# Kernel tuning notes

Hardware: AMD Instinct MI355X
Metric: run time of the kernel (lower is better)

Reference implementation:

```python
import jax, jax.numpy as jnp
import numpy as np

H = 768        # bert hidden_size
HID = 512      # lstm_hidden
HALF = HID // 2
T = 20         # tagset_size
START, STOP = 18, 19
S = 16386      # input positions incl. CLS/SEP
NEG = -10000.0


def setup_inputs() -> dict:
    key = jax.random.key(0)
    ks = jax.random.split(key, 12)
    sc_x = 1.0
    x = jax.random.normal(ks[0], (1, S, H), dtype=jnp.float32)
    # PyTorch LSTM params (gate order i,f,g,o), one layer, bidirectional
    s_ih = 1.0 / np.sqrt(HALF)
    w_ih_f = jax.random.uniform(ks[1], (4 * HALF, H), jnp.float32, -s_ih, s_ih)
    w_hh_f = jax.random.uniform(ks[2], (4 * HALF, HALF), jnp.float32, -s_ih, s_ih)
    b_ih_f = jax.random.uniform(ks[3], (4 * HALF,), jnp.float32, -s_ih, s_ih)
    b_hh_f = jax.random.uniform(ks[4], (4 * HALF,), jnp.float32, -s_ih, s_ih)
    w_ih_b = jax.random.uniform(ks[5], (4 * HALF, H), jnp.float32, -s_ih, s_ih)
    w_hh_b = jax.random.uniform(ks[6], (4 * HALF, HALF), jnp.float32, -s_ih, s_ih)
    b_ih_b = jax.random.uniform(ks[7], (4 * HALF,), jnp.float32, -s_ih, s_ih)
    b_hh_b = jax.random.uniform(ks[8], (4 * HALF,), jnp.float32, -s_ih, s_ih)
    s_t = 1.0 / np.sqrt(HID)
    w_tag = jax.random.uniform(ks[9], (T, HID), jnp.float32, -s_t, s_t)
    b_tag = jax.random.uniform(ks[10], (T,), jnp.float32, -s_t, s_t)
    transitions = jax.random.normal(ks[11], (T, T), dtype=jnp.float32)
    transitions = transitions.at[START, :].set(NEG).at[:, STOP].set(NEG)
    return {
        "x": x,
        "w_ih_f": w_ih_f, "w_hh_f": w_hh_f, "b_ih_f": b_ih_f, "b_hh_f": b_hh_f,
        "w_ih_b": w_ih_b, "w_hh_b": w_hh_b, "b_ih_b": b_ih_b, "b_hh_b": b_hh_b,
        "w_tag": w_tag, "b_tag": b_tag, "transitions": transitions,
    }


def _lstm_one_step(xt, w_ih, b_ih, b_hh):
    # Original passes [1, N, H] to a batch_first=False LSTM => seq_len=1,
    # batch=N, zero initial state. So each token does ONE cell step:
    # h0=c0=0 => hh contribution is only b_hh.
    g = xt @ w_ih.T + b_ih + b_hh          # [N, 4*HALF]
    i, f, gg, o = jnp.split(g, 4, axis=-1)  # PyTorch gate order i,f,g,o
    c = jax.nn.sigmoid(i) * jnp.tanh(gg)    # f*c0 = 0
    return jax.nn.sigmoid(o) * jnp.tanh(c)  # [N, HALF]


def reference(x, w_ih_f, w_hh_f, b_ih_f, b_hh_f,
              w_ih_b, w_hh_b, b_ih_b, b_hh_b,
              w_tag, b_tag, transitions):
    tok = x[0, 1:-1, :]                     # narrow(1,1,S-2): drop CLS/SEP -> [N,H]
    h_f = _lstm_one_step(tok, w_ih_f, b_ih_f, b_hh_f)
    h_b = _lstm_one_step(tok, w_ih_b, b_ih_b, b_hh_b)
    enc = jnp.concatenate([h_f, h_b], axis=-1)   # [N, HID]
    feats = enc @ w_tag.T + b_tag                # [N, T] emission scores

    # ---- Viterbi decode (sequential DP over tokens) ----
    init = jnp.full((T,), NEG, dtype=feats.dtype).at[START].set(0.0)

    def vstep(fv, feat):
        scores = fv[None, :] + transitions       # [next_tag, prev_tag]
        bp = jnp.argmax(scores, axis=1)          # backpointers [T]
        fv_new = jnp.max(scores, axis=1) + feat
        return fv_new, bp

    fv, bps = jax.lax.scan(vstep, init, feats)   # bps: [N, T]
    terminal = fv + transitions[STOP]
    best = jnp.argmax(terminal)
    path_score = terminal[best]

    def btrack(b, bp):
        return bp[b], b                          # emit tag at time t, move to t-1

    _, best_path = jax.lax.scan(btrack, best, bps, reverse=True)  # [N] in time order
    return path_score, best_path
```

## Files before the change

kernel.cpp:

```cpp
#include <hip/hip_runtime.h>
#include <math.h>

#define HDIM 768
#define HIDD 512
#define NTOK 16384
#define NT 20
#define CHUNKS 128
#define CLEN 128

typedef unsigned short ushort_t;
typedef __attribute__((ext_vector_type(8))) short bf16x8;
typedef __attribute__((ext_vector_type(4))) float f32x4;

__device__ __forceinline__ float sigm(float x){ return 1.0f/(1.0f+expf(-x)); }

__device__ __forceinline__ ushort_t f2bf(float f){
    unsigned int u = __float_as_uint(f);
    unsigned int r = (u + 0x7fffu + ((u >> 16) & 1u)) >> 16;
    return (ushort_t)r;
}
__device__ __forceinline__ float bf2f(ushort_t b){
    return __uint_as_float(((unsigned int)b) << 16);
}

#define GLD16(gp, lp) __builtin_amdgcn_global_load_lds( \
    (const __attribute__((address_space(1))) void*)(gp), \
    (__attribute__((address_space(3))) void*)(lp), 16, 0, 0)

__global__ __launch_bounds__(256) void conv_kernel(
    const float* __restrict__ x,
    const float* __restrict__ wf, const float* __restrict__ wb,
    ushort_t* __restrict__ Ah, ushort_t* __restrict__ Al,
    ushort_t* __restrict__ Bh, ushort_t* __restrict__ Bl)
{
    const int bid = blockIdx.x;
    if (bid < 1152){
        int t = bid*256 + threadIdx.x;
        int n = t / 192, c4 = (t - n*192)*4;
        int dir = n / 768, nr = n - dir*768;
        int gate = nr >> 8, j = nr & 255;
        int wrow = j + ((gate==0)?0:((gate==1)?512:768));
        const float* src = dir ? wb : wf;
        const float4 v = *(const float4*)(src + (size_t)wrow*HDIM + c4);
        float f[4] = {v.x, v.y, v.z, v.w};
        ushort_t h[4], l[4];
        #pragma unroll
        for (int i=0;i<4;++i){
            h[i] = f2bf(f[i]);
            l[i] = f2bf(f[i] - bf2f(h[i]));
        }
        *(ushort4*)(Bh + (size_t)n*HDIM + c4) = make_ushort4(h[0],h[1],h[2],h[3]);
        *(ushort4*)(Bl + (size_t)n*HDIM + c4) = make_ushort4(l[0],l[1],l[2],l[3]);
    } else {
        int t = (bid-1152)*256 + threadIdx.x;
        int row = t / 192, c4 = (t - row*192)*4;
        const float4 v = *(const float4*)(x + (size_t)(row+1)*HDIM + c4);
        float f[4] = {v.x, v.y, v.z, v.w};
        ushort_t h[4], l[4];
        #pragma unroll
        for (int i=0;i<4;++i){
            h[i] = f2bf(f[i]);
            l[i] = f2bf(f[i] - bf2f(h[i]));
        }
        *(ushort4*)(Ah + (size_t)row*HDIM + c4) = make_ushort4(h[0],h[1],h[2],h[3]);
        *(ushort4*)(Al + (size_t)row*HDIM + c4) = make_ushort4(l[0],l[1],l[2],l[3]);
    }
}

#define VMCNT(n) asm volatile("s_waitcnt vmcnt(" #n ")" ::: "memory")
#define BARRIER() asm volatile("s_barrier" ::: "memory")
#define LGKM0()  do{ asm volatile("s_waitcnt lgkmcnt(0)" ::: "memory"); \
                     __builtin_amdgcn_sched_barrier(0); }while(0)

#define READ_B(g, ab) do{                                                     \
    bfr[0] = *(const bf16x8*)((ab) + 16384 + (g)*16384 + boffB[0]);           \
    bfr[1] = *(const bf16x8*)((ab) + 16384 + (g)*16384 + 8192 + boffB[0]);    \
    bfr[2] = *(const bf16x8*)((ab) + 16384 + (g)*16384 + boffB[1]);           \
    bfr[3] = *(const bf16x8*)((ab) + 16384 + (g)*16384 + 8192 + boffB[1]);    \
}while(0)

#define READ_AH(S, ab) do{ _Pragma("unroll") for (int f=0; f<4; ++f)          \
    aH##S[f] = *(const bf16x8*)((ab) + aoffB[f]); }while(0)
#define READ_AL(ab) do{ _Pragma("unroll") for (int f=0; f<4; ++f)             \
    aL[f] = *(const bf16x8*)((ab) + 8192 + aoffB[f]); }while(0)

#define MFMA_CLUSTER(g, S) do{                                                \
  __builtin_amdgcn_s_setprio(1);                                              \
  _Pragma("unroll")                                                           \
  for (int fn=0; fn<2; ++fn){                                                 \
    _Pragma("unroll")                                                         \
    for (int fm=0; fm<4; ++fm){                                               \
      acc[g][fm][fn] = __builtin_amdgcn_mfma_f32_16x16x32_bf16(aH##S[fm],     \
          bfr[fn*2], acc[g][fm][fn], 0, 0, 0);                                \
      acc[g][fm][fn] = __builtin_amdgcn_mfma_f32_16x16x32_bf16(aL[fm],        \
          bfr[fn*2], acc[g][fm][fn], 0, 0, 0);                                \
      acc[g][fm][fn] = __builtin_amdgcn_mfma_f32_16x16x32_bf16(aH##S[fm],     \
          bfr[fn*2+1], acc[g][fm][fn], 0, 0, 0);                              \
    }                                                                         \
  }                                                                           \
  __builtin_amdgcn_s_setprio(0);                                              \
  __builtin_amdgcn_sched_barrier(0);                                          \
}while(0)

#define PH0(kt, P, CUR) do{                                                   \
    const int k0n = ((kt)+1)*32;                                              \
    char* abn = smem + (1-(P))*65536;                                         \
    GLD16(Ah + gA + k0n, abn + wbB);                                          \
    GLD16(Al + gA + k0n, abn + 8192 + wbB);                                   \
    GLD16(Bh + gB0 + k0n, abn + 16384 + wbB);                                 \
    GLD16(Bl + gB0 + k0n, abn + 24576 + wbB);                                 \
    VMCNT(8); BARRIER();                                                      \
    const char* ab = smem + (P)*65536;                                        \
    READ_AL(ab);                                                              \
    READ_B(0, ab);                                                            \
    LGKM0();                                                                  \
    MFMA_CLUSTER(0, CUR);                                                     \
}while(0)

#define PH1(kt, P, CUR) do{                                                   \
    const int k0n = ((kt)+1)*32;                                              \
    char* abn = smem + (1-(P))*65536;                                         \
    GLD16(Bh + gB1 + k0n, abn + 32768 + wbB);                                 \
    GLD16(Bl + gB1 + k0n, abn + 40960 + wbB);                                 \
    VMCNT(8); BARRIER();                                                      \
    const char* ab = smem + (P)*65536;                                        \
    READ_B(1, ab);                                                            \
    LGKM0();                                                                  \
    MFMA_CLUSTER(1, CUR);                                                     \
}while(0)

#define PH2(kt, P, CUR, NXT) do{                                              \
    const int k0n = ((kt)+1)*32;                                              \
    char* abn = smem + (1-(P))*65536;                                         \
    GLD16(Bh + gB2 + k0n, abn + 49152 + wbB);                                 \
    GLD16(Bl + gB2 + k0n, abn + 57344 + wbB);                                 \
    VMCNT(4); BARRIER();                                                      \
    const char* ab = smem + (P)*65536;                                        \
    READ_B(2, ab);                                                            \
    READ_AH(NXT, abn);                                                        \
    LGKM0();                                                                  \
    MFMA_CLUSTER(2, CUR);                                                     \
}while(0)

__global__ __launch_bounds__(512, 2) void gemm_fused(
    const ushort_t* __restrict__ Ah, const ushort_t* __restrict__ Al,
    const ushort_t* __restrict__ Bh, const ushort_t* __restrict__ Bl,
    const float* __restrict__ bihf, const float* __restrict__ bhhf,
    const float* __restrict__ bihb, const float* __restrict__ bhhb,
    const float* __restrict__ wtag, float* __restrict__ featsp)
{
    __shared__ __align__(16) char smem[131072];
    float* hbuf = (float*)smem;
    float* wts  = (float*)(smem + 33280);

    const int tid = threadIdx.x;
    const int bx = blockIdx.x;
    const int xcd = bx & 7, g3 = bx >> 3;
    const int qb = g3 & 3, mt = (g3 >> 2)*8 + xcd;
    const int dir = qb >> 1, jhalf = qb & 1;
    const int j0 = jhalf*128;
    const int row0 = mt*128;
    const float* __restrict__ bih = dir ? bihb : bihf;
    const float* __restrict__ bhh = dir ? bhhb : bhhf;

    const int lane = tid & 63, wv = tid >> 6;
    const int wm = wv >> 2, wn = wv & 3;
    const int lm = lane & 15, lq = lane >> 4;
    const int wbB = (tid & 448) * 16;

    const int P_ = tid >> 3, s_ = tid & 7;
    const int q_ = s_ ^ (P_ & 7);
    const int mA = (P_ << 1) | (q_ >> 2);
    const int k8s = q_ & 3;
    const size_t gA  = (size_t)(row0 + mA)*HDIM + k8s*8;
    const size_t gB0 = (size_t)(dir*768 +           j0 + mA)*HDIM + k8s*8;
    const size_t gB1 = (size_t)(dir*768 + 256 +     j0 + mA)*HDIM + k8s*8;
    const size_t gB2 = (size_t)(dir*768 + 512 +     j0 + mA)*HDIM + k8s*8;

    int aoffB[4], boffB[2];
    #pragma unroll
    for (int f=0; f<4; ++f){
        int m = wm*64 + f*16 + lm;
        int rg = m >> 6, r = m & 63;
        aoffB[f] = rg*4096 + ((r>>1)*8 + ((((r&1)<<2)|lq) ^ ((r>>1)&7)))*16;
    }
    #pragma unroll
    for (int f=0; f<2; ++f){
        int n = wn*32 + f*16 + lm;
        int rg = n >> 6, r = n & 63;
        boffB[f] = rg*4096 + ((r>>1)*8 + ((((r&1)<<2)|lq) ^ ((r>>1)&7)))*16;
    }

    f32x4 acc[3][4][2];
    #pragma unroll
    for (int g=0; g<3; ++g)
        #pragma unroll
        for (int fm=0; fm<4; ++fm)
            #pragma unroll
            for (int fn=0; fn<2; ++fn)
                acc[g][fm][fn] = (f32x4){0.f,0.f,0.f,0.f};

    bf16x8 aH0[4], aH1[4], aL[4];
    bf16x8 bfr[4];

    {
        GLD16(Ah + gA, smem + wbB);
        GLD16(Al + gA, smem + 8192 + wbB);
        GLD16(Bh + gB0, smem + 16384 + wbB);
        GLD16(Bl + gB0, smem + 24576 + wbB);
        GLD16(Bh + gB1, smem + 32768 + wbB);
        GLD16(Bl + gB1, smem + 40960 + wbB);
        GLD16(Bh + gB2, smem + 49152 + wbB);
        GLD16(Bl + gB2, smem + 57344 + wbB);
        VMCNT(4); BARRIER();
        READ_AH(0, (const char*)smem);
    }

    #pragma unroll 1
    for (int kt2 = 0; kt2 < 11; ++kt2){
        const int kt = kt2*2;
        PH0(kt,   0, 0); PH1(kt,   0, 0); PH2(kt,   0, 0, 1);
        PH0(kt+1, 1, 1); PH1(kt+1, 1, 1); PH2(kt+1, 1, 1, 0);
    }
    PH0(22, 0, 0); PH1(22, 0, 0); PH2(22, 0, 0, 1);

    {
        const char* ab = smem + 65536;
        VMCNT(4); BARRIER();
        READ_AL(ab);
        READ_B(0, ab);
        LGKM0();
        MFMA_CLUSTER(0, 1);
        VMCNT(2); BARRIER();
        READ_B(1, ab);
        LGKM0();
        MFMA_CLUSTER(1, 1);
        VMCNT(0); BARRIER();
        READ_B(2, ab);
        LGKM0();
        MFMA_CLUSTER(2, 1);
    }

    int jcol[2];
    #pragma unroll
    for (int f=0; f<2; ++f) jcol[f] = j0 + wn*32 + f*16 + lm;

    float bi[2], bg_[2], bo[2];
    #pragma unroll
    for (int f=0; f<2; ++f){
        bi[f]  = bih[jcol[f]]       + bhh[jcol[f]];
        bg_[f] = bih[512 + jcol[f]] + bhh[512 + jcol[f]];
        bo[f]  = bih[768 + jcol[f]] + bhh[768 + jcol[f]];
    }
    float hv[4][2][4];
    #pragma unroll
    for (int fm=0; fm<4; ++fm)
        #pragma unroll
        for (int fn=0; fn<2; ++fn)
            #pragma unroll
            for (int r=0; r<4; ++r){
                float cv = sigm(acc[0][fm][fn][r] + bi[fn]) *
                           tanhf(acc[1][fm][fn][r] + bg_[fn]);
                hv[fm][fn][r] = sigm(acc[2][fm][fn][r] + bo[fn]) * tanhf(cv);
            }

    __syncthreads();
    for (int idx=tid; idx<2*NT*64; idx+=512){
        int cc = idx / (NT*64), r = idx - cc*(NT*64);
        int t = r >> 6, j = r & 63;
        wts[idx] = wtag[t*HIDD + dir*256 + j0 + cc*64 + j];
    }
    #pragma unroll 1
    for (int cc=0; cc<2; ++cc){
        __syncthreads();
        if ((wn >> 1) == cc){
            #pragma unroll
            for (int fm=0; fm<4; ++fm)
                #pragma unroll
                for (int fn=0; fn<2; ++fn)
                    #pragma unroll
                    for (int r=0; r<4; ++r){
                        int mloc = wm*64 + fm*16 + lq*4 + r;
                        int jloc = (wn&1)*32 + fn*16 + lm;
                        hbuf[mloc*65 + jloc] = hv[fm][fn][r];
                    }
        }
        __syncthreads();
        const int mrow = tid & 127, grp = tid >> 7;
        const int tg0 = grp*5;
        const float* wc = wts + cc*(NT*64);
        float s[5] = {0.f,0.f,0.f,0.f,0.f};
        for (int j=0;j<64;++j){
            float h = hbuf[mrow*65 + j];
            #pragma unroll
            for (int tt=0; tt<5; ++tt)
                s[tt] = fmaf(h, wc[(tg0+tt)*64 + j], s[tt]);
        }
        const int p = dir*4 + jhalf*2 + cc;
        float* fq = featsp + (size_t)p * (NTOK*NT);
        const int mglob = row0 + mrow;
        #pragma unroll
        for (int tt=0; tt<5; ++tt)
            fq[(size_t)mglob*NT + tg0 + tt] = s[tt];
    }
}

__device__ __forceinline__ void load_fl(
    const float* __restrict__ featsp, const float* __restrict__ btg,
    float* fl, int c, int tid, int nthr)
{
    const int base = c*(CLEN*NT/4);
    for (int idx=tid; idx<CLEN*NT/4; idx+=nthr){
        float4 s[8];
        #pragma unroll
        for (int p=0; p<8; ++p)
            s[p] = ((const float4*)(featsp + (size_t)p*NTOK*NT))[base+idx];
        float4 v;
        v.x = ((s[0].x+s[1].x)+(s[2].x+s[3].x)) + ((s[4].x+s[5].x)+(s[6].x+s[7].x));
        v.y = ((s[0].y+s[1].y)+(s[2].y+s[3].y)) + ((s[4].y+s[5].y)+(s[6].y+s[7].y));
        v.z = ((s[0].z+s[1].z)+(s[2].z+s[3].z)) + ((s[4].z+s[5].z)+(s[6].z+s[7].z));
        v.w = ((s[0].w+s[1].w)+(s[2].w+s[3].w)) + ((s[4].w+s[5].w)+(s[6].w+s[7].w));
        int t0 = (idx*4) % 20;
        v.x += btg[t0]; v.y += btg[t0+1]; v.z += btg[t0+2]; v.w += btg[t0+3];
        ((float4*)fl)[idx] = v;
    }
}

__global__ __launch_bounds__(512) void vit_chunkmat(
    const float* __restrict__ featsp, const float* __restrict__ btag,
    const float* __restrict__ trans, float* __restrict__ Pall)
{
    __shared__ float fl[CLEN*NT];
    __shared__ float Pb[2][NT*NT];
    const int c = blockIdx.x, tid = threadIdx.x;
    load_fl(featsp, btag, fl, c, tid, 512);
    const bool act = tid < NT*NT;
    const int i = tid/20, j = tid - i*20;
    float tr[NT];
    if (act){
        #pragma unroll
        for (int k=0;k<NT;++k) tr[k] = trans[i*NT+k];
        Pb[0][tid] = (i==j) ? 0.f : -1e30f;
    }
    __syncthreads();
    int cur = 0;
    for (int t=0;t<CLEN;++t){
        float m = -3.0e38f;
        if (act){
            #pragma unroll
            for (int k=0;k<NT;++k) m = fmaxf(m, tr[k] + Pb[cur][k*NT+j]);
            m += fl[t*NT+i];
            Pb[cur^1][tid] = m;
        }
        __syncthreads();
        cur ^= 1;
    }
    if (act) Pall[(size_t)c*(NT*NT) + tid] = Pb[cur][tid];
}

__global__ __launch_bounds__(128) void vit_scan(
    const float* __restrict__ Pall, const float* __restrict__ trans,
    float* __restrict__ fvstart, float* __restrict__ dout, int* __restrict__ bestws)
{
    __shared__ float Pb[NT*NT];
    __shared__ float fv[NT];
    const int tid = threadIdx.x;
    float4 pn = {0.f,0.f,0.f,0.f};
    if (tid<100) pn = ((const float4*)Pall)[tid];
    if (tid<NT) fv[tid] = (tid==18) ? 0.f : -10000.f;
    for (int c=0;c<CHUNKS;++c){
        if (tid<100) ((float4*)Pb)[tid] = pn;
        if (tid<100 && c+1<CHUNKS) pn = ((const float4*)(Pall + (size_t)(c+1)*(NT*NT)))[tid];
        __syncthreads();
        if (tid<NT) fvstart[c*NT+tid] = fv[tid];
        float nf = -3.0e38f;
        if (tid<NT){
            #pragma unroll
            for (int j=0;j<NT;++j) nf = fmaxf(nf, Pb[tid*NT+j] + fv[j]);
        }
        __syncthreads();
        if (tid<NT) fv[tid] = nf;
    }
    __syncthreads();
    if (tid==0){
        float best = -3.0e38f; int bidx = 0;
        for (int j=0;j<NT;++j){
            float tv = fv[j] + trans[19*NT+j];
            if (tv > best){ best = tv; bidx = j; }
        }
        dout[0] = best;
        bestws[0] = bidx;
    }
}

__global__ __launch_bounds__(128) void vit_replay(
    const float* __restrict__ featsp, const float* __restrict__ btag,
    const float* __restrict__ trans, const float* __restrict__ fvstart,
    unsigned int* __restrict__ bpout, int* __restrict__ Hout)
{
    __shared__ float fl[CLEN*NT];
    __shared__ float fv[NT];
    __shared__ unsigned char bp[CLEN*NT];
    const int c = blockIdx.x, tid = threadIdx.x;
    load_fl(featsp, btag, fl, c, tid, 128);
    float tr[NT];
    if (tid<NT){
        fv[tid] = fvstart[c*NT+tid];
        #pragma unroll
        for (int k=0;k<NT;++k) tr[k] = trans[tid*NT+k];
    }
    __syncthreads();
    for (int t=0;t<CLEN;++t){
        float best = 0.f; int bj = 0;
        if (tid<NT){
            best = tr[0] + fv[0];
            #pragma unroll
            for (int j=1;j<NT;++j){
                float v = tr[j] + fv[j];
                if (v > best){ best = v; bj = j; }
            }
        }
        __syncthreads();
        if (tid<NT){
            fv[tid] = best + fl[t*NT+tid];
            bp[t*NT+tid] = (unsigned char)bj;
        }
        __syncthreads();
    }
    for (int idx=tid; idx<CLEN*NT/4; idx+=128)
        bpout[(size_t)c*(CLEN*NT/4) + idx] = ((unsigned int*)bp)[idx];
    if (tid<NT){
        int m = tid;
        for (int t=CLEN-1;t>=0;--t) m = bp[t*NT+m];
        Hout[c*NT+tid] = m;
    }
}

__global__ __launch_bounds__(64) void bt_fill(
    const unsigned int* __restrict__ bpin, const int* __restrict__ Hin,
    const int* __restrict__ bestws, float* __restrict__ dout)
{
    __shared__ int Hl[CHUNKS*NT];
    __shared__ unsigned char bp[CLEN*NT];
    __shared__ float ob[CLEN];
    const int c = blockIdx.x, tid = threadIdx.x;
    for (int idx=tid; idx<CHUNKS*NT; idx+=64) Hl[idx] = Hin[idx];
    for (int idx=tid; idx<CLEN*NT/4; idx+=64)
        ((unsigned int*)bp)[idx] = bpin[(size_t)c*(CLEN*NT/4) + idx];
    __syncthreads();
    if (tid==0){
        int e = bestws[0];
        for (int cc=CHUNKS-1; cc>c; --cc) e = Hl[cc*NT+e];
        for (int t=CLEN-1;t>=0;--t){ ob[t] = (float)e; e = bp[t*NT+e]; }
    }
    __syncthreads();
    for (int idx=tid; idx<CLEN; idx+=64)
        dout[1 + c*CLEN + idx] = ob[idx];
}

extern "C" void kernel_launch(void* const* d_in, const int* in_sizes, int n_in,
                              void* d_out, int out_size, void* d_ws, size_t ws_size,
                              hipStream_t stream)
{
    const float* x    = (const float*)d_in[0];
    const float* wf   = (const float*)d_in[1];
    const float* bihf = (const float*)d_in[3];
    const float* bhhf = (const float*)d_in[4];
    const float* wb   = (const float*)d_in[5];
    const float* bihb = (const float*)d_in[7];
    const float* bhhb = (const float*)d_in[8];
    const float* wtag = (const float*)d_in[9];
    const float* btag = (const float*)d_in[10];
    const float* trans= (const float*)d_in[11];
    float* out = (float*)d_out;

    char* w = (char*)d_ws;
    ushort_t* Ah = (ushort_t*)w;         w += 25165824;
    ushort_t* Al = (ushort_t*)w;         w += 25165824;
    ushort_t* Bh = (ushort_t*)w;         w += 2359296;
    ushort_t* Bl = (ushort_t*)w;         w += 2359296;
    float* featsp = (float*)w;           w += 10485760;
    float* Pall  = (float*)w;            w += 204800;
    float* fvst  = (float*)w;            w += 10240;
    int* Hmap    = (int*)w;              w += 10240;
    unsigned int* bp = (unsigned int*)w; w += 327680;
    int* best    = (int*)w;

    conv_kernel<<<13440, 256, 0, stream>>>(x, wf, wb, Ah, Al, Bh, Bl);
    gemm_fused<<<512, 512, 0, stream>>>(Ah, Al, Bh, Bl, bihf, bhhf, bihb, bhhb,
                                        wtag, featsp);
    vit_chunkmat<<<CHUNKS, 512, 0, stream>>>(featsp, btag, trans, Pall);
    vit_scan<<<1, 128, 0, stream>>>(Pall, trans, fvst, out, best);
    vit_replay<<<CHUNKS, 128, 0, stream>>>(featsp, btag, trans, fvst, bp, Hmap);
    bt_fill<<<CHUNKS, 64, 0, stream>>>(bp, Hmap, best, out);
}
```

Measured before the change: 370.9 us.

## Double-buffer LDS fragment registers to overlap reads with MFMA clusters

Restructures the GEMM main loop so the B fragments (and both A hi/lo fragments) for the next phase are read from shared memory into a second register set while the current MFMA cluster runs. This replaces the explicit lgkmcnt(0) wait before each cluster. It also reorders the global-load issue and vmcnt thresholds so the barrier comes before the next reads. The aim is to hide LDS latency behind matrix math, at the cost of more VGPRs under the 512x2 launch bounds and a possible risk of spills or ordering hazards.

```diff
diff --git a/kernel.cpp b/kernel.cpp
--- a/kernel.cpp
+++ b/kernel.cpp
@@ -69,77 +69,70 @@
 
 #define VMCNT(n) asm volatile("s_waitcnt vmcnt(" #n ")" ::: "memory")
 #define BARRIER() asm volatile("s_barrier" ::: "memory")
-#define LGKM0()  do{ asm volatile("s_waitcnt lgkmcnt(0)" ::: "memory"); \
-                     __builtin_amdgcn_sched_barrier(0); }while(0)
-
-#define READ_B(g, ab) do{                                                     \
-    bfr[0] = *(const bf16x8*)((ab) + 16384 + (g)*16384 + boffB[0]);           \
-    bfr[1] = *(const bf16x8*)((ab) + 16384 + (g)*16384 + 8192 + boffB[0]);    \
-    bfr[2] = *(const bf16x8*)((ab) + 16384 + (g)*16384 + boffB[1]);           \
-    bfr[3] = *(const bf16x8*)((ab) + 16384 + (g)*16384 + 8192 + boffB[1]);    \
+
+#define READ_B(S, g, ab) do{                                                  \
+    bfr##S[0] = *(const bf16x8*)((ab) + 16384 + (g)*16384 + boffB[0]);        \
+    bfr##S[1] = *(const bf16x8*)((ab) + 16384 + (g)*16384 + 8192 + boffB[0]); \
+    bfr##S[2] = *(const bf16x8*)((ab) + 16384 + (g)*16384 + boffB[1]);        \
+    bfr##S[3] = *(const bf16x8*)((ab) + 16384 + (g)*16384 + 8192 + boffB[1]); \
 }while(0)
 
-#define READ_AH(S, ab) do{ _Pragma("unroll") for (int f=0; f<4; ++f)          \
-    aH##S[f] = *(const bf16x8*)((ab) + aoffB[f]); }while(0)
-#define READ_AL(ab) do{ _Pragma("unroll") for (int f=0; f<4; ++f)             \
-    aL[f] = *(const bf16x8*)((ab) + 8192 + aoffB[f]); }while(0)
-
-#define MFMA_CLUSTER(g, S) do{                                                \
+#define READ_A2(S, ab) do{ _Pragma("unroll") for (int f=0; f<4; ++f){         \
+    aH##S[f] = *(const bf16x8*)((ab) + aoffB[f]);                             \
+    aL##S[f] = *(const bf16x8*)((ab) + 8192 + aoffB[f]); } }while(0)
+
+#define MFMA_CLUSTER(g, AS, BS) do{                                           \
+  __builtin_amdgcn_sched_barrier(0);                                          \
   __builtin_amdgcn_s_setprio(1);                                              \
   _Pragma("unroll")                                                           \
   for (int fn=0; fn<2; ++fn){                                                 \
     _Pragma("unroll")                                                         \
     for (int fm=0; fm<4; ++fm){                                               \
-      acc[g][fm][fn] = __builtin_amdgcn_mfma_f32_16x16x32_bf16(aH##S[fm],     \
-          bfr[fn*2], acc[g][fm][fn], 0, 0, 0);                                \
-      acc[g][fm][fn] = __builtin_amdgcn_mfma_f32_16x16x32_bf16(aL[fm],        \
-          bfr[fn*2], acc[g][fm][fn], 0, 0, 0);                                \
-      acc[g][fm][fn] = __builtin_amdgcn_mfma_f32_16x16x32_bf16(aH##S[fm],     \
-          bfr[fn*2+1], acc[g][fm][fn], 0, 0, 0);                              \
+      acc[g][fm][fn] = __builtin_amdgcn_mfma_f32_16x16x32_bf16(aH##AS[fm],    \
+          bfr##BS[fn*2], acc[g][fm][fn], 0, 0, 0);                            \
+      acc[g][fm][fn] = __builtin_amdgcn_mfma_f32_16x16x32_bf16(aL##AS[fm],    \
+          bfr##BS[fn*2], acc[g][fm][fn], 0, 0, 0);                            \
+      acc[g][fm][fn] = __builtin_amdgcn_mfma_f32_16x16x32_bf16(aH##AS[fm],    \
+          bfr##BS[fn*2+1], acc[g][fm][fn], 0, 0, 0);                          \
     }                                                                         \
   }                                                                           \
   __builtin_amdgcn_s_setprio(0);                                              \
   __builtin_amdgcn_sched_barrier(0);                                          \
 }while(0)
 
-#define PH0(kt, P, CUR) do{                                                   \
+#define PH0(kt, P, AC, BC, BR) do{                                            \
     const int k0n = ((kt)+1)*32;                                              \
     char* abn = smem + (1-(P))*65536;                                         \
+    const char* ab = smem + (P)*65536;                                        \
+    VMCNT(2); BARRIER();                                                      \
+    READ_B(BR, 1, ab);                                                        \
     GLD16(Ah + gA + k0n, abn + wbB);                                          \
     GLD16(Al + gA + k0n, abn + 8192 + wbB);                                   \
     GLD16(Bh + gB0 + k0n, abn + 16384 + wbB);                                 \
     GLD16(Bl + gB0 + k0n, abn + 24576 + wbB);                                 \
-    VMCNT(8); BARRIER();                                                      \
-    const char* ab = smem + (P)*65536;                                        \
-    READ_AL(ab);                                                              \
-    READ_B(0, ab);                                                            \
-    LGKM0();                                                                  \
-    MFMA_CLUSTER(0, CUR);                                                     \
+    MFMA_CLUSTER(0, AC, BC);                                                  \
 }while(0)
 
-#define PH1(kt, P, CUR) do{                                                   \
+#define PH1(kt, P, AC, BC, BR) do{                                            \
     const int k0n = ((kt)+1)*32;                                              \
     char* abn = smem + (1-(P))*65536;                                         \
+    const char* ab = smem + (P)*65536;                                        \
+    VMCNT(4); BARRIER();                                                      \
+    READ_B(BR, 2, ab);                                                        \
     GLD16(Bh + gB1 + k0n, abn + 32768 + wbB);                                 \
     GLD16(Bl + gB1 + k0n, abn + 40960 + wbB);                                 \
-    VMCNT(8); BARRIER();                                                      \
-    const char* ab = smem + (P)*65536;                                        \
-    READ_B(1, ab);                                                            \
-    LGKM0();                                                                  \
-    MFMA_CLUSTER(1, CUR);                                                     \
+    MFMA_CLUSTER(1, AC, BC);                                                  \
 }while(0)
 
-#define PH2(kt, P, CUR, NXT) do{                                              \
+#define PH2(kt, P, AC, BC, BR, AN) do{                                        \
     const int k0n = ((kt)+1)*32;                                              \
     char* abn = smem + (1-(P))*65536;                                         \
+    VMCNT(2); BARRIER();                                                      \
+    READ_A2(AN, abn);                                                         \
+    READ_B(BR, 0, abn);                                                       \
     GLD16(Bh + gB2 + k0n, abn + 49152 + wbB);                                 \
     GLD16(Bl + gB2 + k0n, abn + 57344 + wbB);                                 \
-    VMCNT(4); BARRIER();                                                      \
-    const char* ab = smem + (P)*65536;                                        \
-    READ_B(2, ab);                                                            \
-    READ_AH(NXT, abn);                                                        \
-    LGKM0();                                                                  \
-    MFMA_CLUSTER(2, CUR);                                                     \
+    MFMA_CLUSTER(2, AC, BC);                                                  \
 }while(0)
 
 __global__ __launch_bounds__(512, 2) void gemm_fused(
@@ -200,8 +193,8 @@
             for (int fn=0; fn<2; ++fn)
                 acc[g][fm][fn] = (f32x4){0.f,0.f,0.f,0.f};
 
-    bf16x8 aH0[4], aH1[4], aL[4];
-    bf16x8 bfr[4];
+    bf16x8 aH0[4], aL0[4], aH1[4], aL1[4];
+    bf16x8 bfrA[4], bfrB[4];
 
     {
         GLD16(Ah + gA, smem + wbB);
@@ -213,32 +206,27 @@
         GLD16(Bh + gB2, smem + 49152 + wbB);
         GLD16(Bl + gB2, smem + 57344 + wbB);
         VMCNT(4); BARRIER();
-        READ_AH(0, (const char*)smem);
+        READ_A2(0, (const char*)smem);
+        READ_B(A, 0, (const char*)smem);
     }
 
     #pragma unroll 1
     for (int kt2 = 0; kt2 < 11; ++kt2){
         const int kt = kt2*2;
-        PH0(kt,   0, 0); PH1(kt,   0, 0); PH2(kt,   0, 0, 1);
-        PH0(kt+1, 1, 1); PH1(kt+1, 1, 1); PH2(kt+1, 1, 1, 0);
-    }
-    PH0(22, 0, 0); PH1(22, 0, 0); PH2(22, 0, 0, 1);
+        PH0(kt,   0, 0, A, B); PH1(kt,   0, 0, B, A); PH2(kt,   0, 0, A, B, 1);
+        PH0(kt+1, 1, 1, B, A); PH1(kt+1, 1, 1, A, B); PH2(kt+1, 1, 1, B, A, 0);
+    }
+    PH0(22, 0, 0, A, B); PH1(22, 0, 0, B, A); PH2(22, 0, 0, A, B, 1);
 
     {
         const char* ab = smem + 65536;
-        VMCNT(4); BARRIER();
-        READ_AL(ab);
-        READ_B(0, ab);
-        LGKM0();
-        MFMA_CLUSTER(0, 1);
         VMCNT(2); BARRIER();
-        READ_B(1, ab);
-        LGKM0();
-        MFMA_CLUSTER(1, 1);
+        READ_B(A, 1, ab);
+        MFMA_CLUSTER(0, 1, B);
         VMCNT(0); BARRIER();
-        READ_B(2, ab);
-        LGKM0();
-        MFMA_CLUSTER(2, 1);
+        READ_B(B, 2, ab);
+        MFMA_CLUSTER(1, 1, A);
+        MFMA_CLUSTER(2, 1, B);
     }
 
     int jcol[2];
```

Result: no change. 371.0 us (+0.0%).
